# Performance work log

Hardware: AMD Instinct MI355X
Metric: run time of the kernel (lower is better)

The kernel has to match this reference:

```python
import jax, jax.numpy as jnp
import numpy as np

N, E = 50000, 800000
DIN, FIN, H, DN, FE = 128, 7, 4, 64, 32
NEG_SLOPE = 0.01  # torch leaky_relu default


def setup_inputs() -> dict:
    key = jax.random.key(0)
    ks = jax.random.split(key, 8)
    nfeats = jax.random.normal(ks[0], (N, DIN), dtype=jnp.float32)
    efeats = jax.random.uniform(ks[1], (E, FIN), dtype=jnp.float32)
    src = jax.random.randint(ks[2], (E,), 0, N, dtype=jnp.int32)
    dst = jax.random.randint(ks[3], (E,), 0, N, dtype=jnp.int32)
    # parameters (xavier-normal-ish scale), stored in jax [in, out] layout
    W_nodes = jax.random.normal(ks[4], (DIN, H * DN), dtype=jnp.float32) * (2.0 / (DIN + H * DN)) ** 0.5
    b_nodes = jnp.zeros((H * DN,), dtype=jnp.float32)
    W_edges = jax.random.normal(ks[5], (FIN + 2 * DIN, H * FE), dtype=jnp.float32) * (2.0 / (FIN + 2 * DIN + H * FE)) ** 0.5
    W_attn = jax.random.normal(ks[6], (H, FE), dtype=jnp.float32) * (2.0 / (FE + H)) ** 0.5  # torch [out,in] layout
    return {"nfeats": nfeats, "efeats": efeats, "src": src, "dst": dst,
            "W_nodes": W_nodes, "b_nodes": b_nodes, "W_edges": W_edges, "W_attn": W_attn}


def reference(nfeats, efeats, src, dst, W_nodes, b_nodes, W_edges, W_attn):
    n = nfeats.shape[0]
    e = efeats.shape[0]
    h_heads = W_attn.shape[0]
    # node projection: [N, H, DN]
    h = (nfeats @ W_nodes + b_nodes).reshape(n, h_heads, -1)
    # per-edge feature MLP on [h_src || f || h_dst]  (raw node feats, as in edge_attention)
    stack = jnp.concatenate([nfeats[src], efeats, nfeats[dst]], axis=-1)  # [E, FIN+2*DIN]
    f_out = jax.nn.leaky_relu(stack @ W_edges, NEG_SLOPE).reshape(e, h_heads, -1)  # [E, H, FE]
    # a = fc_attn(f_out).sum(-1): sums over both attn output heads and FE
    a = jnp.einsum('ehj,kj->eh', f_out, W_attn)  # [E, H]
    # segment (per-destination) softmax, numerically stable
    amax = jax.ops.segment_max(a, dst, num_segments=n)          # [N, H]
    ex = jnp.exp(a - amax[dst])                                 # [E, H]
    denom = jax.ops.segment_sum(ex, dst, num_segments=n)       # [N, H]
    alpha = ex / denom[dst]                                     # [E, H]
    # weighted aggregation of projected src features
    msg = alpha[:, :, None] * h[src]                            # [E, H, DN]
    h_out = jax.ops.segment_sum(msg, dst, num_segments=n)      # [N, H, DN]
    return h_out, f_out
```

## Files before the change

### kernel.cpp

```cpp
#include <hip/hip_runtime.h>

#define NEG_SLOPE 0.01f

typedef __attribute__((ext_vector_type(8))) __bf16 bf16x8;
typedef __attribute__((ext_vector_type(4))) float  f32x4;

__device__ __forceinline__ unsigned short f2bf(float x) {
    unsigned u; __builtin_memcpy(&u, &x, 4);
    unsigned r = u + 0x7FFFu + ((u >> 16) & 1u);
    return (unsigned short)(r >> 16);
}
__device__ __forceinline__ float bflo(unsigned u) {
    unsigned v = u << 16; float f; __builtin_memcpy(&f, &v, 4); return f;
}
__device__ __forceinline__ float bfhi(unsigned u) {
    unsigned v = u & 0xFFFF0000u; float f; __builtin_memcpy(&f, &v, 4); return f;
}

__device__ __forceinline__ void stream_store8(void* p, unsigned long long v) {
    asm volatile("global_store_dwordx2 %0, %1, off sc0 sc1 nt"
                 :: "v"((unsigned long long)(__UINTPTR_TYPE__)p), "v"(v) : "memory");
}
__device__ __forceinline__ void stream_store16(void* p, f32x4 v) {
    asm volatile("global_store_dwordx4 %0, %1, off sc0 sc1 nt"
                 :: "v"((unsigned long long)(__UINTPTR_TYPE__)p), "v"(v) : "memory");
}

__global__ void zero_kernel(int* __restrict__ p, int n) {
    int i = blockIdx.x * blockDim.x + threadIdx.x;
    if (i < n) p[i] = 0;
}

__global__ __launch_bounds__(256) void bt_prep(
    const float* __restrict__ Wn, const float* __restrict__ We,
    short* __restrict__ Btg)
{
    int idx = blockIdx.x * 256 + threadIdx.x;
    int n = idx >> 7, k = idx & 127;
    float v;
    if (n < 256)      v = Wn[(size_t)k * 256 + n];
    else if (n < 384) v = We[(size_t)k * 128 + (n - 256)];
    else              v = We[(size_t)(135 + k) * 128 + (n - 384)];
    Btg[(size_t)n * 128 + k] = (short)f2bf(v);
}

__global__ __launch_bounds__(256) void gemm_mfma(
    const float* __restrict__ A, const float* __restrict__ bn,
    const short* __restrict__ Btg, unsigned short* __restrict__ PH,
    unsigned short* __restrict__ Qbf, int N)
{
    __shared__ __align__(16) short Al[64 * 136];
    __shared__ __align__(16) short Bl[128 * 136];
    int t = threadIdx.x;
    int ct = blockIdx.y;
    int row0 = blockIdx.x * 64;

    #pragma unroll
    for (int i = 0; i < 8; i++) {
        int idx = t + i * 256;
        int fr = idx >> 5, fc4 = idx & 31;
        int row = row0 + fr;
        float4 v = make_float4(0.f, 0.f, 0.f, 0.f);
        if (row < N) v = *(const float4*)(A + (size_t)row * 128 + fc4 * 4);
        unsigned long long pk =  (unsigned long long)f2bf(v.x)
                              | ((unsigned long long)f2bf(v.y) << 16)
                              | ((unsigned long long)f2bf(v.z) << 32)
                              | ((unsigned long long)f2bf(v.w) << 48);
        *(unsigned long long*)&Al[fr * 136 + fc4 * 4] = pk;
    }
    #pragma unroll
    for (int i = 0; i < 8; i++) {
        int idx = t + i * 256;
        int r = idx >> 4, c8 = idx & 15;
        uint4 v = *(const uint4*)(Btg + (size_t)(ct * 128 + r) * 128 + c8 * 8);
        *(uint4*)&Bl[r * 136 + c8 * 8] = v;
    }
    __syncthreads();

    int w = t >> 6, l = t & 63;
    int lr = l & 15, lg = l >> 4;

    f32x4 acc[8];
    #pragma unroll
    for (int fc = 0; fc < 8; fc++) {
        acc[fc][0] = 0.f; acc[fc][1] = 0.f; acc[fc][2] = 0.f; acc[fc][3] = 0.f;
    }

    #pragma unroll
    for (int ks = 0; ks < 4; ks++) {
        int k0 = ks * 32 + lg * 8;
        bf16x8 a0 = *(const bf16x8*)&Al[(w * 16 + lr) * 136 + k0];
        #pragma unroll
        for (int fc = 0; fc < 8; fc++) {
            bf16x8 bb = *(const bf16x8*)&Bl[(fc * 16 + lr) * 136 + k0];
            acc[fc] = __builtin_amdgcn_mfma_f32_16x16x32_bf16(a0, bb, acc[fc], 0, 0, 0);
        }
    }

    #pragma unroll
    for (int fc = 0; fc < 8; fc++) {
        int col = fc * 16 + lr;
        float bias = (ct < 2) ? bn[ct * 128 + col] : 0.f;
        #pragma unroll
        for (int b = 0; b < 4; b++) {
            int row = row0 + w * 16 + lg * 4 + b;
            if (row >= N) continue;
            unsigned short bv = f2bf(acc[fc][b] + bias);
            if (ct < 2) {
                int col256 = ct * 128 + col;
                PH[(size_t)row * 384 + (col256 >> 2) * 6 + 2 + (col256 & 3)] = bv;
            } else if (ct == 2) {
                PH[(size_t)row * 384 + (col >> 1) * 6 + (col & 1)] = bv;
            } else {
                Qbf[(size_t)row * 128 + col] = bv;
            }
        }
    }
}

__global__ void count_kernel(const int* __restrict__ dst, int* __restrict__ deg, int E) {
    int i = blockIdx.x * blockDim.x + threadIdx.x;
    if (i < E) atomicAdd(&deg[dst[i]], 1);
}

__global__ __launch_bounds__(256) void scan_sum(
    const int* __restrict__ deg, int* __restrict__ bsum, int n)
{
    int b = blockIdx.x, t = threadIdx.x;
    int base = b * 1024 + t * 4;
    int s = 0;
    #pragma unroll
    for (int k = 0; k < 4; k++) { int i = base + k; if (i < n) s += deg[i]; }
    #pragma unroll
    for (int off = 32; off >= 1; off >>= 1) s += __shfl_xor(s, off);
    __shared__ int ws[4];
    if ((t & 63) == 0) ws[t >> 6] = s;
    __syncthreads();
    if (t == 0) bsum[b] = ws[0] + ws[1] + ws[2] + ws[3];
}

__global__ void scan_offsets(const int* __restrict__ bsum, int* __restrict__ boff,
                             int nb, int* __restrict__ row_start, int n)
{
    int acc = 0;
    for (int b = 0; b < nb; b++) { boff[b] = acc; acc += bsum[b]; }
    row_start[n] = acc;
}

__global__ __launch_bounds__(256) void scan_write(
    const int* __restrict__ deg, const int* __restrict__ boff,
    int* __restrict__ row_start, int* __restrict__ cursor, int n)
{
    int b = blockIdx.x, t = threadIdx.x, lane = t & 63, w = t >> 6;
    int base = b * 1024 + t * 4;
    int x0, x1, x2, x3;
    x0 = (base + 0 < n) ? deg[base + 0] : 0;
    x1 = (base + 1 < n) ? deg[base + 1] : 0;
    x2 = (base + 2 < n) ? deg[base + 2] : 0;
    x3 = (base + 3 < n) ? deg[base + 3] : 0;
    int tsum = x0 + x1 + x2 + x3;
    int inc = tsum;
    #pragma unroll
    for (int off = 1; off < 64; off <<= 1) {
        int v = __shfl_up(inc, off);
        if (lane >= off) inc += v;
    }
    int texcl = inc - tsum;
    __shared__ int wsum[4];
    if (lane == 63) wsum[w] = inc;
    __syncthreads();
    int wexcl = 0;
    #pragma unroll
    for (int ww = 0; ww < 4; ww++) if (ww < w) wexcl += wsum[ww];
    int basev = boff[b] + wexcl + texcl;
    int p0 = basev;
    int p1 = p0 + x0;
    int p2 = p1 + x1;
    int p3 = p2 + x2;
    if (base + 0 < n) { row_start[base + 0] = p0; cursor[base + 0] = p0; }
    if (base + 1 < n) { row_start[base + 1] = p1; cursor[base + 1] = p1; }
    if (base + 2 < n) { row_start[base + 2] = p2; cursor[base + 2] = p2; }
    if (base + 3 < n) { row_start[base + 3] = p3; cursor[base + 3] = p3; }
}

__global__ void scatter_kernel(const int* __restrict__ dst, const int* __restrict__ src,
                               int* __restrict__ cursor, int2* __restrict__ es, int E) {
    int i = blockIdx.x * blockDim.x + threadIdx.x;
    if (i < E) {
        int pos = atomicAdd(&cursor[dst[i]], 1);
        es[pos] = make_int2(i, src[i]);
    }
}

__global__ __launch_bounds__(256) void fused_kernel(
    const int* __restrict__ row_start, const int2* __restrict__ ES,
    const float* __restrict__ ef,
    const unsigned short* __restrict__ PH, const unsigned short* __restrict__ Qbf,
    const float* __restrict__ We, const float* __restrict__ Wa,
    float* __restrict__ f_out, float* __restrict__ out, int N)
{
    int t = threadIdx.x;
    int lane = t & 63;
    int n = (int)((blockIdx.x * blockDim.x + t) >> 6);
    if (n >= N) return;
    int c0 = lane * 2;

    float* Obase = out + (size_t)n * 256 + lane * 4;
    int nu = __builtin_amdgcn_readfirstlane(n);
    int start = row_start[nu];
    int deg   = row_start[nu + 1] - start;
    if (deg == 0) {
        f32x4 z; z[0] = 0.f; z[1] = 0.f; z[2] = 0.f; z[3] = 0.f;
        stream_store16(Obase, z);
        return;
    }

    float wf0[7], wf1[7];
    #pragma unroll
    for (int j = 0; j < 7; j++) {
        wf0[j] = We[(size_t)(128 + j) * 128 + c0];
        wf1[j] = We[(size_t)(128 + j) * 128 + c0 + 1];
    }
    int j0 = c0 & 31, j1 = j0 + 1;
    float wv0 = Wa[j0] + Wa[32 + j0] + Wa[64 + j0] + Wa[96 + j0];
    float wv1 = Wa[j1] + Wa[32 + j1] + Wa[64 + j1] + Wa[96 + j1];

    unsigned qu = ((const unsigned*)Qbf)[(size_t)n * 64 + lane];
    float q0 = bflo(qu), q1 = bfhi(qu);

    #define DSTR(X) \
        float m##X = -1e30f, d##X = 0.f;                                  \
        float4 a##X = make_float4(0.f, 0.f, 0.f, 0.f);                    \
        int e##X = 0; unsigned pu##X = 0; uint2 hu##X = make_uint2(0u,0u);\
        float f##X##0=0.f,f##X##1=0.f,f##X##2=0.f,f##X##3=0.f,            \
              f##X##4=0.f,f##X##5=0.f,f##X##6=0.f;
    #define DNXT(X) \
        int e##X = 0; unsigned pu##X = 0; uint2 hu##X = make_uint2(0u,0u);\
        float f##X##0=0.f,f##X##1=0.f,f##X##2=0.f,f##X##3=0.f,            \
              f##X##4=0.f,f##X##5=0.f,f##X##6=0.f;

    #define LOADE(pos, X) {                                               \
        int p_ = start + (pos);                                           \
        int2 es_ = ES[p_];                                                \
        e##X = __builtin_amdgcn_readfirstlane(es_.x);                     \
        int s_ = __builtin_amdgcn_readfirstlane(es_.y);                   \
        uint3 ph_ = *(const uint3*)(PH + (size_t)s_ * 384 + lane * 6);    \
        pu##X = ph_.x;                                                    \
        hu##X = make_uint2(ph_.y, ph_.z);                                 \
        const float* ep_ = ef + (size_t)e##X * 7;                         \
        f##X##0 = ep_[0]; f##X##1 = ep_[1]; f##X##2 = ep_[2];             \
        f##X##3 = ep_[3]; f##X##4 = ep_[4]; f##X##5 = ep_[5];             \
        f##X##6 = ep_[6]; }

    #define PROC(X) {                                                     \
        float a0 = bflo(pu##X) + q0, a1 = bfhi(pu##X) + q1;               \
        a0 = fmaf(f##X##0, wf0[0], a0); a1 = fmaf(f##X##0, wf1[0], a1);   \
        a0 = fmaf(f##X##1, wf0[1], a0); a1 = fmaf(f##X##1, wf1[1], a1);   \
        a0 = fmaf(f##X##2, wf0[2], a0); a1 = fmaf(f##X##2, wf1[2], a1);   \
        a0 = fmaf(f##X##3, wf0[3], a0); a1 = fmaf(f##X##3, wf1[3], a1);   \
        a0 = fmaf(f##X##4, wf0[4], a0); a1 = fmaf(f##X##4, wf1[4], a1);   \
        a0 = fmaf(f##X##5, wf0[5], a0); a1 = fmaf(f##X##5, wf1[5], a1);   \
        a0 = fmaf(f##X##6, wf0[6], a0); a1 = fmaf(f##X##6, wf1[6], a1);   \
        float v0 = a0 > 0.f ? a0 : NEG_SLOPE * a0;                        \
        float v1 = a1 > 0.f ? a1 : NEG_SLOPE * a1;                        \
        float2 fv_ = make_float2(v0, v1);                                 \
        unsigned long long u_;                                            \
        __builtin_memcpy(&u_, &fv_, 8);                                   \
        stream_store8(f_out + (size_t)e##X * 128 + c0, u_);               \
        float p_ = fmaf(v0, wv0, v1 * wv1);                               \
        p_ += __shfl_xor(p_, 8);                                          \
        p_ += __shfl_xor(p_, 4);                                          \
        p_ += __shfl_xor(p_, 2);                                          \
        p_ += __shfl_xor(p_, 1);                                          \
        float nm_ = fmaxf(m##X, p_);                                      \
        float sc_ = __expf(m##X - nm_);                                   \
        float pe_ = __expf(p_ - nm_);                                     \
        d##X = d##X * sc_ + pe_;                                          \
        float hx0 = bflo(hu##X.x), hx1 = bfhi(hu##X.x);                   \
        float hx2 = bflo(hu##X.y), hx3 = bfhi(hu##X.y);                   \
        a##X.x = fmaf(a##X.x, sc_, pe_ * hx0);                            \
        a##X.y = fmaf(a##X.y, sc_, pe_ * hx1);                            \
        a##X.z = fmaf(a##X.z, sc_, pe_ * hx2);                            \
        a##X.w = fmaf(a##X.w, sc_, pe_ * hx3);                            \
        m##X = nm_; }

    #define ROT(X, Y) { e##X = e##Y; pu##X = pu##Y; hu##X = hu##Y;        \
        f##X##0 = f##Y##0; f##X##1 = f##Y##1; f##X##2 = f##Y##2;          \
        f##X##3 = f##Y##3; f##X##4 = f##Y##4; f##X##5 = f##Y##5;          \
        f##X##6 = f##Y##6; }

    DSTR(A) DSTR(B) DSTR(C) DSTR(D)

    LOADE(0, A);
    if (deg > 1) LOADE(1, B);
    if (deg > 2) LOADE(2, C);
    if (deg > 3) LOADE(3, D);

    for (int k = 0;; k++) {
        int base = 4 * k;
        DNXT(An) DNXT(Bn) DNXT(Cn) DNXT(Dn)
        if (base + 4 < deg) LOADE(base + 4, An);
        if (base + 5 < deg) LOADE(base + 5, Bn);
        if (base + 6 < deg) LOADE(base + 6, Cn);
        if (base + 7 < deg) LOADE(base + 7, Dn);

        PROC(A);
        if (base + 1 < deg) PROC(B);
        if (base + 2 < deg) PROC(C);
        if (base + 3 < deg) PROC(D);

        if (base + 4 >= deg) break;
        ROT(A, An); ROT(B, Bn); ROT(C, Cn); ROT(D, Dn);
    }

    float nm = fmaxf(fmaxf(mA, mB), fmaxf(mC, mD));
    float scA = __expf(mA - nm), scB = __expf(mB - nm);
    float scC = __expf(mC - nm), scD = __expf(mD - nm);
    float den = dA * scA + dB * scB + dC * scC + dD * scD;
    float r = 1.f / den;
    f32x4 acc;
    acc[0] = (aA.x * scA + aB.x * scB + aC.x * scC + aD.x * scD) * r;
    acc[1] = (aA.y * scA + aB.y * scB + aC.y * scC + aD.y * scD) * r;
    acc[2] = (aA.z * scA + aB.z * scB + aC.z * scC + aD.z * scD) * r;
    acc[3] = (aA.w * scA + aB.w * scB + aC.w * scC + aD.w * scD) * r;
    stream_store16(Obase, acc);

    #undef DSTR
    #undef DNXT
    #undef LOADE
    #undef PROC
    #undef ROT
}

extern "C" void kernel_launch(void* const* d_in, const int* in_sizes, int n_in,
                              void* d_out, int out_size, void* d_ws, size_t ws_size,
                              hipStream_t stream)
{
    const float* nfeats = (const float*)d_in[0];
    const float* efeats = (const float*)d_in[1];
    const int*   src    = (const int*)d_in[2];
    const int*   dst    = (const int*)d_in[3];
    const float* Wn     = (const float*)d_in[4];
    const float* bn     = (const float*)d_in[5];
    const float* We     = (const float*)d_in[6];
    const float* Wa     = (const float*)d_in[7];

    int N = in_sizes[0] / 128;
    int E = in_sizes[2];

    char* ws = (char*)d_ws;
    size_t off = 0;
    unsigned short* PH  = (unsigned short*)(ws + off); off += (size_t)N * 384 * 2;
    unsigned short* Qbf = (unsigned short*)(ws + off); off += (size_t)N * 128 * 2;
    short* Btg   = (short*)(ws + off); off += (size_t)512 * 128 * 2;
    int2* es       = (int2*)(ws + off); off += (size_t)E * 8;
    int* deg       = (int*)(ws + off); off += (size_t)(N + 1) * 4;
    int* row_start = (int*)(ws + off); off += (size_t)(N + 1) * 4;
    int* cursor    = (int*)(ws + off); off += (size_t)(N + 1) * 4;
    int* bsum      = (int*)(ws + off); off += 1024;
    int* boff      = (int*)(ws + off); off += 1024;

    float* h_out = (float*)d_out;
    float* f_out = (float*)d_out + (size_t)N * 256;

    zero_kernel<<<(N + 255) / 256, 256, 0, stream>>>(deg, N);

    bt_prep<<<256, 256, 0, stream>>>(Wn, We, Btg);

    dim3 g2((N + 63) / 64, 4);
    gemm_mfma<<<g2, 256, 0, stream>>>(nfeats, bn, Btg, PH, Qbf, N);

    count_kernel<<<(E + 255) / 256, 256, 0, stream>>>(dst, deg, E);

    int nb = (N + 1023) / 1024;
    scan_sum<<<nb, 256, 0, stream>>>(deg, bsum, N);
    scan_offsets<<<1, 1, 0, stream>>>(bsum, boff, nb, row_start, N);
    scan_write<<<nb, 256, 0, stream>>>(deg, boff, row_start, cursor, N);

    scatter_kernel<<<(E + 255) / 256, 256, 0, stream>>>(dst, src, cursor, es, E);

    fused_kernel<<<(N + 3) / 4, 256, 0, stream>>>(row_start, es, efeats,
                                                  PH, Qbf, We, Wa,
                                                  f_out, h_out, N);
}
```

Baseline: 331.6 us.

## Record per-edge atomic rank during counting to remove second atomic scatter pass

The counting kernel now saves each edge's local rank within its destination (the atomicAdd return value) as a 16-bit value. The scatter kernel then computes each slot as row_start plus that rank, so it needs no second round of atomics and no cursor array. The single-thread scan_offsets launch is folded into scan_write, where each block sums the preceding block totals itself. This removes one kernel launch and the atomic contention in scatter, at the cost of an extra E*2-byte write and read, and it assumes no node has more than 65535 incoming edges.

```diff
diff --git a/kernel.cpp b/kernel.cpp
--- a/kernel.cpp
+++ b/kernel.cpp
@@ -118,9 +118,10 @@
     }
 }
 
-__global__ void count_kernel(const int* __restrict__ dst, int* __restrict__ deg, int E) {
+__global__ void scatter1_kernel(const int* __restrict__ dst, int* __restrict__ deg,
+                                unsigned short* __restrict__ tmp, int E) {
     int i = blockIdx.x * blockDim.x + threadIdx.x;
-    if (i < E) atomicAdd(&deg[dst[i]], 1);
+    if (i < E) tmp[i] = (unsigned short)atomicAdd(&deg[dst[i]], 1);
 }
 
 __global__ __launch_bounds__(256) void scan_sum(
@@ -139,19 +140,20 @@
     if (t == 0) bsum[b] = ws[0] + ws[1] + ws[2] + ws[3];
 }
 
-__global__ void scan_offsets(const int* __restrict__ bsum, int* __restrict__ boff,
-                             int nb, int* __restrict__ row_start, int n)
-{
-    int acc = 0;
-    for (int b = 0; b < nb; b++) { boff[b] = acc; acc += bsum[b]; }
-    row_start[n] = acc;
-}
-
 __global__ __launch_bounds__(256) void scan_write(
-    const int* __restrict__ deg, const int* __restrict__ boff,
-    int* __restrict__ row_start, int* __restrict__ cursor, int n)
+    const int* __restrict__ deg, const int* __restrict__ bsum,
+    int* __restrict__ row_start, int n, int nb)
 {
     int b = blockIdx.x, t = threadIdx.x, lane = t & 63, w = t >> 6;
+    __shared__ int boff_s;
+    if (t == 0) {
+        int a = 0;
+        for (int j = 0; j < b; j++) a += bsum[j];
+        boff_s = a;
+        if (b == nb - 1) row_start[n] = a + bsum[b];
+    }
+    __syncthreads();
+
     int base = b * 1024 + t * 4;
     int x0, x1, x2, x3;
     x0 = (base + 0 < n) ? deg[base + 0] : 0;
@@ -172,22 +174,23 @@
     int wexcl = 0;
     #pragma unroll
     for (int ww = 0; ww < 4; ww++) if (ww < w) wexcl += wsum[ww];
-    int basev = boff[b] + wexcl + texcl;
-    int p0 = basev;
+    int p0 = boff_s + wexcl + texcl;
     int p1 = p0 + x0;
     int p2 = p1 + x1;
     int p3 = p2 + x2;
-    if (base + 0 < n) { row_start[base + 0] = p0; cursor[base + 0] = p0; }
-    if (base + 1 < n) { row_start[base + 1] = p1; cursor[base + 1] = p1; }
-    if (base + 2 < n) { row_start[base + 2] = p2; cursor[base + 2] = p2; }
-    if (base + 3 < n) { row_start[base + 3] = p3; cursor[base + 3] = p3; }
-}
-
-__global__ void scatter_kernel(const int* __restrict__ dst, const int* __restrict__ src,
-                               int* __restrict__ cursor, int2* __restrict__ es, int E) {
+    if (base + 0 < n) row_start[base + 0] = p0;
+    if (base + 1 < n) row_start[base + 1] = p1;
+    if (base + 2 < n) row_start[base + 2] = p2;
+    if (base + 3 < n) row_start[base + 3] = p3;
+}
+
+__global__ void scatter2_kernel(const int* __restrict__ dst, const int* __restrict__ src,
+                                const int* __restrict__ row_start,
+                                const unsigned short* __restrict__ tmp,
+                                int2* __restrict__ es, int E) {
     int i = blockIdx.x * blockDim.x + threadIdx.x;
     if (i < E) {
-        int pos = atomicAdd(&cursor[dst[i]], 1);
+        int pos = row_start[dst[i]] + (int)tmp[i];
         es[pos] = make_int2(i, src[i]);
     }
 }
@@ -354,11 +357,10 @@
     unsigned short* Qbf = (unsigned short*)(ws + off); off += (size_t)N * 128 * 2;
     short* Btg   = (short*)(ws + off); off += (size_t)512 * 128 * 2;
     int2* es       = (int2*)(ws + off); off += (size_t)E * 8;
+    unsigned short* tmp = (unsigned short*)(ws + off); off += (size_t)E * 2;
     int* deg       = (int*)(ws + off); off += (size_t)(N + 1) * 4;
     int* row_start = (int*)(ws + off); off += (size_t)(N + 1) * 4;
-    int* cursor    = (int*)(ws + off); off += (size_t)(N + 1) * 4;
     int* bsum      = (int*)(ws + off); off += 1024;
-    int* boff      = (int*)(ws + off); off += 1024;
 
     float* h_out = (float*)d_out;
     float* f_out = (float*)d_out + (size_t)N * 256;
@@ -370,14 +372,13 @@
     dim3 g2((N + 63) / 64, 4);
     gemm_mfma<<<g2, 256, 0, stream>>>(nfeats, bn, Btg, PH, Qbf, N);
 
-    count_kernel<<<(E + 255) / 256, 256, 0, stream>>>(dst, deg, E);
+    scatter1_kernel<<<(E + 255) / 256, 256, 0, stream>>>(dst, deg, tmp, E);
 
     int nb = (N + 1023) / 1024;
     scan_sum<<<nb, 256, 0, stream>>>(deg, bsum, N);
-    scan_offsets<<<1, 1, 0, stream>>>(bsum, boff, nb, row_start, N);
-    scan_write<<<nb, 256, 0, stream>>>(deg, boff, row_start, cursor, N);
-
-    scatter_kernel<<<(E + 255) / 256, 256, 0, stream>>>(dst, src, cursor, es, E);
+    scan_write<<<nb, 256, 0, stream>>>(deg, bsum, row_start, N, nb);
+
+    scatter2_kernel<<<(E + 255) / 256, 256, 0, stream>>>(dst, src, row_start, tmp, es, E);
 
     fused_kernel<<<(N + 3) / 4, 256, 0, stream>>>(row_start, es, efeats,
                                                   PH, Qbf, We, Wa,
```

Result: faster. 295.5 us (-10.9%).
